# Kernel tuning notes

Measured on AMD Instinct MI355X. Metric: run time of the kernel, lower is better.

## Reference

```python
import jax, jax.numpy as jnp
import numpy as np

N = 100000   # total nodes in batched graph
E = 600000   # total edges
B = 64       # graphs in batch
H = 128      # hidden_dim
A = 64       # action_dim
L = 4        # num mpnn layers
LOG_STD_MIN, LOG_STD_MAX = -20.0, 2.0


def setup_inputs() -> dict:
    key = jax.random.key(0)
    ks = jax.random.split(key, 40)
    s = 0.05

    def w(k, shape):
        return (jax.random.normal(k, shape, jnp.float32) * s)

    inp = {}
    inp["node_feat"] = jax.random.normal(ks[0], (N, 7), jnp.float32)
    inp["edge_feat"] = jax.random.normal(ks[1], (E, 2), jnp.float32)
    # node encoder: Linear(7,H) -> ReLU -> Linear(H,H)
    inp["ne_w1"] = w(ks[2], (7, H)); inp["ne_b1"] = jnp.zeros((H,), jnp.float32)
    inp["ne_w2"] = w(ks[3], (H, H)); inp["ne_b2"] = jnp.zeros((H,), jnp.float32)
    # edge encoder: Linear(2,H) -> ReLU -> Linear(H,H)
    inp["ee_w1"] = w(ks[4], (2, H)); inp["ee_b1"] = jnp.zeros((H,), jnp.float32)
    inp["ee_w2"] = w(ks[5], (H, H)); inp["ee_b2"] = jnp.zeros((H,), jnp.float32)
    # per-layer message net: Linear(3H,H) -> ReLU -> Linear(H,H)  (stacked over L)
    inp["msg_w1"] = w(ks[6], (L, 3 * H, H)); inp["msg_b1"] = jnp.zeros((L, H), jnp.float32)
    inp["msg_w2"] = w(ks[7], (L, H, H));     inp["msg_b2"] = jnp.zeros((L, H), jnp.float32)
    # per-layer update net: Linear(2H,H) -> ReLU -> Linear(H,H)
    inp["upd_w1"] = w(ks[8], (L, 2 * H, H)); inp["upd_b1"] = jnp.zeros((L, H), jnp.float32)
    inp["upd_w2"] = w(ks[9], (L, H, H));     inp["upd_b2"] = jnp.zeros((L, H), jnp.float32)
    # attention-pooling gate: Linear(H,H) -> ReLU -> Linear(H,1)
    inp["gate_w1"] = w(ks[10], (H, H)); inp["gate_b1"] = jnp.zeros((H,), jnp.float32)
    inp["gate_w2"] = w(ks[11], (H, 1)); inp["gate_b2"] = jnp.zeros((1,), jnp.float32)
    # policy net: Linear(H,H) -> ReLU -> Linear(H,H) -> ReLU -> Linear(H,2A)
    inp["pol_w1"] = w(ks[12], (H, H));     inp["pol_b1"] = jnp.zeros((H,), jnp.float32)
    inp["pol_w2"] = w(ks[13], (H, H));     inp["pol_b2"] = jnp.zeros((H,), jnp.float32)
    inp["pol_w3"] = w(ks[14], (H, 2 * A)); inp["pol_b3"] = jnp.zeros((2 * A,), jnp.float32)
    # graph connectivity
    inp["src"] = jax.random.randint(ks[15], (E,), 0, N)
    inp["dst"] = jax.random.randint(ks[16], (E,), 0, N)
    inp["graph_id"] = jnp.sort(jax.random.randint(ks[17], (N,), 0, B))
    return inp


def _mlp2(x, w1, b1, w2, b2):
    return jax.nn.relu(x @ w1 + b1) @ w2 + b2


def reference(node_feat, edge_feat,
              ne_w1, ne_b1, ne_w2, ne_b2,
              ee_w1, ee_b1, ee_w2, ee_b2,
              msg_w1, msg_b1, msg_w2, msg_b2,
              upd_w1, upd_b1, upd_w2, upd_b2,
              gate_w1, gate_b1, gate_w2, gate_b2,
              pol_w1, pol_b1, pol_w2, pol_b2, pol_w3, pol_b3,
              src, dst, graph_id):
    # encode
    h = _mlp2(node_feat, ne_w1, ne_b1, ne_w2, ne_b2)          # [N, H]
    e = _mlp2(edge_feat, ee_w1, ee_b1, ee_w2, ee_b2)          # [E, H]
    # MPNN layers with residual (h = layer(h) + h)
    for l in range(L):
        msg_in = jnp.concatenate([h[src], h[dst], e], axis=1)  # [E, 3H]
        m = _mlp2(msg_in, msg_w1[l], msg_b1[l], msg_w2[l], msg_b2[l])  # [E, H]
        h_agg = jax.ops.segment_sum(m, dst, num_segments=N)    # [N, H]
        upd_in = jnp.concatenate([h, h_agg], axis=1)           # [N, 2H]
        h = _mlp2(upd_in, upd_w1[l], upd_b1[l], upd_w2[l], upd_b2[l]) + h
    # global attention pooling (per-graph segment softmax over gate logits)
    gate = _mlp2(h, gate_w1, gate_b1, gate_w2, gate_b2)[:, 0]  # [N]
    gmax = jax.ops.segment_max(gate, graph_id, num_segments=B)  # [B]
    ex = jnp.exp(gate - gmax[graph_id])                        # [N]
    z = jax.ops.segment_sum(ex, graph_id, num_segments=B)      # [B]
    alpha = ex / z[graph_id]                                   # [N]
    emb = jax.ops.segment_sum(alpha[:, None] * h, graph_id, num_segments=B)  # [B, H]
    # policy head
    out = jax.nn.relu(jax.nn.relu(emb @ pol_w1 + pol_b1) @ pol_w2 + pol_b2) @ pol_w3 + pol_b3  # [B, 2A]
    mean, log_std = out[:, :A], out[:, A:]
    log_std = jnp.clip(log_std, LOG_STD_MIN, LOG_STD_MAX)
    std = jnp.exp(log_std)
    return (mean, std)
```

## Files before the change

kernel.cpp:

```cpp
#include <hip/hip_runtime.h>
#include <stdint.h>

#define NN 100000
#define NE 600000
#define NG 64
#define HD 128
#define HD2 (HD*HD)
#define NLAYER 4
#define SCAN_NB 391
#define NTILES ((NN + 63) / 64)
#define PSLICE 16

typedef unsigned short u16;
typedef unsigned int u32;
typedef unsigned long long u64;
typedef __attribute__((ext_vector_type(8))) short bf16x8;
typedef __attribute__((ext_vector_type(4))) float f32x4;

__device__ __forceinline__ float bf2f(u32 v) { return __uint_as_float(v << 16); }
__device__ __forceinline__ u16 f2bf(float f) {
    u32 u = __float_as_uint(f);
    return (u16)((u + 0x7FFFu + ((u >> 16) & 1u)) >> 16);
}
__device__ __forceinline__ u32 pk2(float a, float b) {
    return (u32)f2bf(a) | ((u32)f2bf(b) << 16);
}

template<bool RELU, bool GATE>
__global__ __launch_bounds__(256, 3) void mgemm_kernel(
    const u16* __restrict__ Xb, const u16* __restrict__ Wt,
    const float* __restrict__ bias, const float* __restrict__ degscale,
    const u16* __restrict__ addend, u16* __restrict__ out, int M,
    const float* __restrict__ gw2, const float* __restrict__ gb2,
    float* __restrict__ gate)
{
    __shared__ u16 WsL[HD * HD];
    __shared__ u16 XsL[64 * HD];
    const int t = threadIdx.x;
    const int lane = t & 63, wave = t >> 6;
    const int cj = ((lane >> 4) << 2);

    for (int i = t; i < HD * 16; i += 256) {
        const int row = i >> 4, c16 = i & 15;
        uint4 v = *(const uint4*)(Wt + (size_t)row * HD + c16 * 8);
        *(uint4*)((char*)WsL + (((row << 8) + (c16 << 4)) ^ ((row & 7) << 4))) = v;
    }
    float4 bcol[8];
    #pragma unroll
    for (int ct = 0; ct < 8; ct++)
        bcol[ct] = bias ? *(const float4*)(bias + ct * 16 + cj)
                        : make_float4(0.f, 0.f, 0.f, 0.f);
    float4 gwv[8];
    if (GATE) {
        #pragma unroll
        for (int ct = 0; ct < 8; ct++)
            gwv[ct] = *(const float4*)(gw2 + ct * 16 + cj);
    }

    const int arow = wave * 16 + (lane & 15);
    const int alin = (arow << 8) + ((lane >> 4) << 4);
    const int axor = (arow & 7) << 4;
    __syncthreads();

    for (int tile = blockIdx.x; tile < NTILES; tile += gridDim.x) {
        const int r0 = tile << 6;
        for (int i = t; i < 64 * 16; i += 256) {
            const int row = i >> 4, c16 = i & 15;
            const int rg = r0 + row;
            uint4 v = make_uint4(0, 0, 0, 0);
            if (rg < M) v = *(const uint4*)(Xb + (size_t)rg * HD + c16 * 8);
            *(uint4*)((char*)XsL + (((row << 8) + (c16 << 4)) ^ ((row & 7) << 4))) = v;
        }
        __syncthreads();

        bf16x8 a[4];
        #pragma unroll
        for (int ks = 0; ks < 4; ks++)
            a[ks] = *(const bf16x8*)((const char*)XsL + ((alin + ks * 64) ^ axor));

        f32x4 acc[8];
        #pragma unroll
        for (int ct = 0; ct < 8; ct++) {
            acc[ct][0] = 0.f; acc[ct][1] = 0.f; acc[ct][2] = 0.f; acc[ct][3] = 0.f;
        }
        #pragma unroll
        for (int ct = 0; ct < 8; ct++) {
            const int bn = ct * 16 + (lane & 15);
            #pragma unroll
            for (int ks = 0; ks < 4; ks++) {
                bf16x8 breg = *(const bf16x8*)((const char*)WsL +
                    (((bn << 8) + ks * 64 + ((lane >> 4) << 4)) ^ ((bn & 7) << 4)));
                acc[ct] = __builtin_amdgcn_mfma_f32_16x16x32_bf16(breg, a[ks], acc[ct], 0, 0, 0);
            }
        }

        const int orow = r0 + wave * 16 + (lane & 15);
        const bool rv = orow < M;
        float gdot = 0.f;
        const float ds = (degscale && rv) ? degscale[orow] : 1.f;
        #pragma unroll
        for (int ct = 0; ct < 8; ct++) {
            const int c0 = ct * 16 + cj;
            float v0 = acc[ct][0], v1 = acc[ct][1], v2 = acc[ct][2], v3 = acc[ct][3];
            if (bias) {
                v0 += bcol[ct].x * ds; v1 += bcol[ct].y * ds;
                v2 += bcol[ct].z * ds; v3 += bcol[ct].w * ds;
            }
            if (addend && rv) {
                ushort4 av = *(const ushort4*)(addend + (size_t)orow * HD + c0);
                v0 += bf2f(av.x); v1 += bf2f(av.y); v2 += bf2f(av.z); v3 += bf2f(av.w);
            }
            if (RELU) {
                v0 = fmaxf(v0, 0.f); v1 = fmaxf(v1, 0.f);
                v2 = fmaxf(v2, 0.f); v3 = fmaxf(v3, 0.f);
            }
            if (GATE) {
                gdot += v0 * gwv[ct].x + v1 * gwv[ct].y + v2 * gwv[ct].z + v3 * gwv[ct].w;
            } else if (rv) {
                ushort4 pk;
                pk.x = f2bf(v0); pk.y = f2bf(v1); pk.z = f2bf(v2); pk.w = f2bf(v3);
                *(ushort4*)(out + (size_t)orow * HD + c0) = pk;
            }
        }
        if (GATE) {
            gdot += __shfl_xor(gdot, 16, 64);
            gdot += __shfl_xor(gdot, 32, 64);
            if ((lane >> 4) == 0 && rv) gate[orow] = gdot + gb2[0];
        }
        __syncthreads();
    }
}

__global__ __launch_bounds__(256, 2) void pqgemm_kernel(
    const u16* __restrict__ Xb, const u16* __restrict__ WtP,
    const u16* __restrict__ WtQ, u16* __restrict__ outP,
    u16* __restrict__ outQ, int M)
{
    __shared__ u16 WsL[2 * HD * HD];
    __shared__ u16 XsL[64 * HD];
    const int t = threadIdx.x;
    const int lane = t & 63, wave = t >> 6;
    const int cj = ((lane >> 4) << 2);

    for (int i = t; i < 2 * HD * 16; i += 256) {
        const int w = i >> 11;
        const int j = i & 2047;
        const int row = j >> 4, c16 = j & 15;
        const u16* Wt = w ? WtQ : WtP;
        uint4 v = *(const uint4*)(Wt + (size_t)row * HD + c16 * 8);
        *(uint4*)((char*)WsL + w * 32768 +
                  (((row << 8) + (c16 << 4)) ^ ((row & 7) << 4))) = v;
    }

    const int arow = wave * 16 + (lane & 15);
    const int alin = (arow << 8) + ((lane >> 4) << 4);
    const int axor = (arow & 7) << 4;
    __syncthreads();

    for (int tile = blockIdx.x; tile < NTILES; tile += gridDim.x) {
        const int r0 = tile << 6;
        for (int i = t; i < 64 * 16; i += 256) {
            const int row = i >> 4, c16 = i & 15;
            const int rg = r0 + row;
            uint4 v = make_uint4(0, 0, 0, 0);
            if (rg < M) v = *(const uint4*)(Xb + (size_t)rg * HD + c16 * 8);
            *(uint4*)((char*)XsL + (((row << 8) + (c16 << 4)) ^ ((row & 7) << 4))) = v;
        }
        __syncthreads();

        bf16x8 a[4];
        #pragma unroll
        for (int ks = 0; ks < 4; ks++)
            a[ks] = *(const bf16x8*)((const char*)XsL + ((alin + ks * 64) ^ axor));

        const int orow = r0 + wave * 16 + (lane & 15);
        const bool rv = orow < M;

        #pragma unroll
        for (int o = 0; o < 2; o++) {
            f32x4 acc[8];
            #pragma unroll
            for (int ct = 0; ct < 8; ct++) {
                acc[ct][0] = 0.f; acc[ct][1] = 0.f; acc[ct][2] = 0.f; acc[ct][3] = 0.f;
            }
            #pragma unroll
            for (int ct = 0; ct < 8; ct++) {
                const int bn = ct * 16 + (lane & 15);
                #pragma unroll
                for (int ks = 0; ks < 4; ks++) {
                    bf16x8 breg = *(const bf16x8*)((const char*)WsL + o * 32768 +
                        (((bn << 8) + ks * 64 + ((lane >> 4) << 4)) ^ ((bn & 7) << 4)));
                    acc[ct] = __builtin_amdgcn_mfma_f32_16x16x32_bf16(breg, a[ks], acc[ct], 0, 0, 0);
                }
            }
            if (rv) {
                u16* out = o ? outQ : outP;
                #pragma unroll
                for (int ct = 0; ct < 8; ct++) {
                    ushort4 pk;
                    pk.x = f2bf(acc[ct][0]); pk.y = f2bf(acc[ct][1]);
                    pk.z = f2bf(acc[ct][2]); pk.w = f2bf(acc[ct][3]);
                    *(ushort4*)(out + (size_t)orow * HD + ct * 16 + cj) = pk;
                }
            }
        }
        __syncthreads();
    }
}

__global__ __launch_bounds__(256, 2) void edge_mfma_kernel(
    const float2* __restrict__ sef, const int* __restrict__ ssrc,
    const int* __restrict__ sdst, const int* __restrict__ off,
    const float* __restrict__ ew1, const float* __restrict__ eb1,
    const u16* __restrict__ Mt, const float* __restrict__ mvec,
    const u16* __restrict__ P, const u16* __restrict__ Q,
    u16* __restrict__ agg)
{
    __shared__ __align__(16) char XHT[HD * 72 * 2];
    __shared__ u16 PsL[64 * 136];
    __shared__ u16 QsL[32 * 136];
    __shared__ u64 dlocL[8];
    __shared__ float ew1L[2 * HD];
    __shared__ float eb1L[HD];
    u16* HT = (u16*)XHT;
    const int t = threadIdx.x, lane = t & 63, wave = t >> 6;
    const int cj = (lane >> 4) << 2;
    const int n0 = blockIdx.x * 32;

    ew1L[t] = ew1[t];
    if (t < HD) eb1L[t] = eb1[t];
    for (int i = t; i < 32 * 32; i += 256) {
        const int row = i >> 5, c4 = (i & 31) * 4;
        *(ushort4*)(QsL + row * 136 + c4) = *(const ushort4*)(Q + (size_t)(n0 + row) * HD + c4);
    }

    float4 mvv[8];
    #pragma unroll
    for (int ct = 0; ct < 8; ct++) mvv[ct] = *(const float4*)(mvec + ct * 16 + cj);

    bf16x8 breg[8][4];
    #pragma unroll
    for (int ct = 0; ct < 8; ct++) {
        const int bn = ct * 16 + (lane & 15);
        #pragma unroll
        for (int ks = 0; ks < 4; ks++)
            breg[ct][ks] = *(const bf16x8*)(Mt + (size_t)bn * HD + ks * 32 + ((lane >> 4) << 3));
    }

    const int rt = wave & 1;
    const int c2b = (wave >> 1) * 4;
    const int nodeid = rt * 16 + (lane & 15);
    f32x4 acc2[4];
    #pragma unroll
    for (int i = 0; i < 4; i++) {
        acc2[i][0] = 0.f; acc2[i][1] = 0.f; acc2[i][2] = 0.f; acc2[i][3] = 0.f;
    }

    const int e0 = off[n0], e1 = off[n0 + 32];
    const int arow = wave * 16 + (lane & 15);
    const int alin = (arow << 8) + ((lane >> 4) << 4);
    const int axor = (arow & 7) << 4;
    const int el = wave * 16 + (lane & 15);
    __syncthreads();

    for (int base = e0; base < e1; base += 64) {
        for (int i = t; i < 64 * 16; i += 256) {
            const int row = i >> 4, c16 = i & 15;
            const int e = base + row;
            uint4 v = make_uint4(0, 0, 0, 0);
            uint4 pvv = make_uint4(0, 0, 0, 0);
            if (e < e1) {
                const float2 f = sef[e];
                const int c8 = c16 * 8;
                float o[8];
                #pragma unroll
                for (int k = 0; k < 8; k++)
                    o[k] = fmaxf(f.x * ew1L[c8 + k] + f.y * ew1L[HD + c8 + k] + eb1L[c8 + k], 0.f);
                v = make_uint4(pk2(o[0], o[1]), pk2(o[2], o[3]), pk2(o[4], o[5]), pk2(o[6], o[7]));
                const int srcI = ssrc[e];
                pvv = *(const uint4*)(P + (size_t)srcI * HD + c16 * 8);
            }
            *(uint4*)(XHT + (((row << 8) + (c16 << 4)) ^ ((row & 7) << 4))) = v;
            *(uint4*)(PsL + row * 136 + c16 * 8) = pvv;
        }
        if (t < 64) {
            const int e = base + t;
            ((unsigned char*)dlocL)[t] = (e < e1) ? (unsigned char)(sdst[e] - n0) : (unsigned char)0xFF;
        }
        __syncthreads();

        bf16x8 a[4];
        #pragma unroll
        for (int ks = 0; ks < 4; ks++)
            a[ks] = *(const bf16x8*)(XHT + ((alin + ks * 64) ^ axor));
        const int e = base + el;
        const bool ev = e < e1;
        const int dl = ev ? (int)((const unsigned char*)dlocL)[el] : 0;
        __syncthreads();

        f32x4 acc[8];
        #pragma unroll
        for (int ct = 0; ct < 8; ct++) {
            acc[ct][0] = 0.f; acc[ct][1] = 0.f; acc[ct][2] = 0.f; acc[ct][3] = 0.f;
        }
        #pragma unroll
        for (int ct = 0; ct < 8; ct++)
            #pragma unroll
            for (int ks = 0; ks < 4; ks++)
                acc[ct] = __builtin_amdgcn_mfma_f32_16x16x32_bf16(breg[ct][ks], a[ks], acc[ct], 0, 0, 0);

        #pragma unroll
        for (int ct = 0; ct < 8; ct++) {
            float v0 = 0.f, v1 = 0.f, v2 = 0.f, v3 = 0.f;
            if (ev) {
                const ushort4 pvc = *(const ushort4*)(PsL + el * 136 + ct * 16 + cj);
                const ushort4 qvc = *(const ushort4*)(QsL + dl * 136 + ct * 16 + cj);
                v0 = fmaxf(acc[ct][0] + bf2f(pvc.x) + bf2f(qvc.x) + mvv[ct].x, 0.f);
                v1 = fmaxf(acc[ct][1] + bf2f(pvc.y) + bf2f(qvc.y) + mvv[ct].y, 0.f);
                v2 = fmaxf(acc[ct][2] + bf2f(pvc.z) + bf2f(qvc.z) + mvv[ct].z, 0.f);
                v3 = fmaxf(acc[ct][3] + bf2f(pvc.w) + bf2f(qvc.w) + mvv[ct].w, 0.f);
            }
            const int c0 = ct * 16 + cj;
            HT[(c0 + 0) * 72 + el] = f2bf(v0);
            HT[(c0 + 1) * 72 + el] = f2bf(v1);
            HT[(c0 + 2) * 72 + el] = f2bf(v2);
            HT[(c0 + 3) * 72 + el] = f2bf(v3);
        }
        __syncthreads();

        #pragma unroll
        for (int ks2 = 0; ks2 < 2; ks2++) {
            const u64 dv = dlocL[ks2 * 4 + (lane >> 4)];
            bf16x8 sfrag;
            #pragma unroll
            for (int j = 0; j < 8; j++) {
                const int dvj = (int)((dv >> (8 * j)) & 0xFF);
                sfrag[j] = (dvj == nodeid) ? (short)0x3F80 : (short)0;
            }
            #pragma unroll
            for (int i = 0; i < 4; i++) {
                const int col = (c2b + i) * 16 + (lane & 15);
                bf16x8 hfrag = *(const bf16x8*)(HT + col * 72 + ks2 * 32 + ((lane >> 4) << 3));
                acc2[i] = __builtin_amdgcn_mfma_f32_16x16x32_bf16(sfrag, hfrag, acc2[i], 0, 0, 0);
            }
        }
        __syncthreads();
    }

    u16* BNC = (u16*)XHT;
    #pragma unroll
    for (int i = 0; i < 4; i++) {
        const int col = (c2b + i) * 16 + (lane & 15);
        #pragma unroll
        for (int r = 0; r < 4; r++) {
            const int nl = rt * 16 + ((lane >> 4) << 2) + r;
            BNC[nl * 136 + col] = f2bf(acc2[i][r]);
        }
    }
    __syncthreads();
    for (int i = t; i < 32 * 16; i += 256) {
        const int row = i >> 4, c16 = i & 15;
        *(uint4*)(agg + (size_t)(n0 + row) * HD + c16 * 8) =
            *(const uint4*)(BNC + row * 136 + c16 * 8);
    }
}

__global__ __launch_bounds__(256) void gemm128_kernel(
    const float* __restrict__ X, const float* __restrict__ W,
    float* __restrict__ out, int M)
{
    __shared__ float Ws[HD * HD];
    __shared__ float Xs[32 * HD];
    const int t = threadIdx.x;
    for (int i = t; i < HD * HD / 4; i += 256)
        ((float4*)Ws)[i] = ((const float4*)W)[i];
    const int c0 = (t & 31) * 4;
    const int rb = (t >> 5) * 4;
    __syncthreads();
    const int ntiles = M / 32;
    for (int tile = blockIdx.x; tile < ntiles; tile += gridDim.x) {
        const int r0 = tile * 32;
        const float4* xg = (const float4*)(X + (size_t)r0 * HD);
        for (int i = t; i < 32 * HD / 4; i += 256)
            ((float4*)Xs)[i] = xg[i];
        __syncthreads();
        float acc[4][4];
        #pragma unroll
        for (int a = 0; a < 4; a++)
            #pragma unroll
            for (int b = 0; b < 4; b++) acc[a][b] = 0.f;
        for (int k = 0; k < HD; k += 4) {
            float4 w0 = *(const float4*)(Ws + (k + 0) * HD + c0);
            float4 w1 = *(const float4*)(Ws + (k + 1) * HD + c0);
            float4 w2 = *(const float4*)(Ws + (k + 2) * HD + c0);
            float4 w3 = *(const float4*)(Ws + (k + 3) * HD + c0);
            #pragma unroll
            for (int rr = 0; rr < 4; rr++) {
                float4 xv = *(const float4*)(Xs + (rb + rr) * HD + k);
                acc[rr][0] += xv.x * w0.x + xv.y * w1.x + xv.z * w2.x + xv.w * w3.x;
                acc[rr][1] += xv.x * w0.y + xv.y * w1.y + xv.z * w2.y + xv.w * w3.y;
                acc[rr][2] += xv.x * w0.z + xv.y * w1.z + xv.z * w2.z + xv.w * w3.z;
                acc[rr][3] += xv.x * w0.w + xv.y * w1.w + xv.z * w2.w + xv.w * w3.w;
            }
        }
        #pragma unroll
        for (int rr = 0; rr < 4; rr++) {
            const int row = r0 + rb + rr;
            *(float4*)(out + (size_t)row * HD + c0) =
                make_float4(acc[rr][0], acc[rr][1], acc[rr][2], acc[rr][3]);
        }
        __syncthreads();
    }
}

__global__ void mvec_kernel(const float* __restrict__ eb2,
                            const float* __restrict__ W1c,
                            const float* __restrict__ mb1,
                            float* __restrict__ out) {
    const int j = threadIdx.x;
    if (j < HD) {
        float s = mb1[j];
        for (int i = 0; i < HD; i++) s += eb2[i] * W1c[(size_t)i * HD + j];
        out[j] = s;
    }
}

__global__ __launch_bounds__(256) void wprep_kernel(
    const float* __restrict__ msg_w1, const float* __restrict__ msg_w2,
    const float* __restrict__ upd_w1, const float* __restrict__ upd_w2,
    const float* __restrict__ gw1, const float* __restrict__ ne_w2,
    const float* __restrict__ Mw, u16* __restrict__ wt)
{
    __shared__ float tileL[HD * (HD + 1)];
    const int b = blockIdx.x, t = threadIdx.x;
    const int l = b & 3;
    const float* S;
    if (b < 4)       S = msg_w1 + (size_t)l * 3 * HD2;
    else if (b < 8)  S = msg_w1 + (size_t)l * 3 * HD2 + HD2;
    else if (b < 12) S = Mw + (size_t)l * HD2;
    else if (b < 16) S = msg_w2 + (size_t)l * HD2;
    else if (b < 20) S = upd_w1 + (size_t)l * 2 * HD2;
    else if (b < 24) S = upd_w1 + (size_t)l * 2 * HD2 + HD2;
    else if (b < 28) S = upd_w2 + (size_t)l * HD2;
    else if (b == 28) S = gw1;
    else             S = ne_w2;
    u16* D = wt + (size_t)b * HD2;
    for (int i = t; i < HD2; i += 256) {
        const int k = i >> 7, n = i & 127;
        tileL[k * (HD + 1) + n] = S[i];
    }
    __syncthreads();
    for (int i = t; i < HD2; i += 256) {
        const int n = i >> 7, k = i & 127;
        D[i] = f2bf(tileL[k * (HD + 1) + n]);
    }
}

__global__ __launch_bounds__(256) void ne1_kernel(
    const float* __restrict__ nf, const float* __restrict__ w1,
    const float* __restrict__ b1, u16* __restrict__ out)
{
    __shared__ float w1s[7 * HD];
    __shared__ float b1s[HD];
    const int t = threadIdx.x;
    for (int i = t; i < 7 * HD; i += 256) w1s[i] = w1[i];
    if (t < HD) b1s[t] = b1[t];
    __syncthreads();
    const int row = blockIdx.x * 32 + (t >> 3);
    const int c0 = (t & 7) * 16;
    if (row < NN) {
        float f[7];
        #pragma unroll
        for (int k = 0; k < 7; k++) f[k] = nf[(size_t)row * 7 + k];
        float o[16];
        #pragma unroll
        for (int c = 0; c < 16; c++) {
            float a = b1s[c0 + c];
            #pragma unroll
            for (int k = 0; k < 7; k++) a += f[k] * w1s[k * HD + c0 + c];
            o[c] = fmaxf(a, 0.f);
        }
        uint4 v0 = make_uint4(pk2(o[0], o[1]), pk2(o[2], o[3]), pk2(o[4], o[5]), pk2(o[6], o[7]));
        uint4 v1 = make_uint4(pk2(o[8], o[9]), pk2(o[10], o[11]), pk2(o[12], o[13]), pk2(o[14], o[15]));
        *(uint4*)(out + (size_t)row * HD + c0) = v0;
        *(uint4*)(out + (size_t)row * HD + c0 + 8) = v1;
    }
}

__global__ void deg_count_kernel(const int* __restrict__ dst, int* __restrict__ deg) {
    const int i = blockIdx.x * 256 + threadIdx.x;
    if (i < NE) atomicAdd(&deg[dst[i]], 1);
}
__global__ void scan1_kernel(const int* __restrict__ deg, int* __restrict__ part) {
    __shared__ int s[256];
    const int t = threadIdx.x, i = blockIdx.x * 256 + t;
    s[t] = (i < NN) ? deg[i] : 0;
    __syncthreads();
    for (int d = 128; d > 0; d >>= 1) { if (t < d) s[t] += s[t + d]; __syncthreads(); }
    if (t == 0) part[blockIdx.x] = s[0];
}
__global__ void scan2_kernel(int* __restrict__ part, int nb) {
    if (threadIdx.x == 0 && blockIdx.x == 0) {
        int run = 0;
        for (int b = 0; b < nb; b++) { const int v = part[b]; part[b] = run; run += v; }
    }
}
__global__ void scan3_kernel(const int* __restrict__ deg, const int* __restrict__ part,
                             int* __restrict__ off, int* __restrict__ pos) {
    __shared__ int s[256];
    const int t = threadIdx.x, i = blockIdx.x * 256 + t;
    const int v = (i < NN) ? deg[i] : 0;
    s[t] = v;
    __syncthreads();
    for (int d = 1; d < 256; d <<= 1) {
        const int x = (t >= d) ? s[t - d] : 0;
        __syncthreads();
        s[t] += x;
        __syncthreads();
    }
    const int excl = s[t] - v + part[blockIdx.x];
    if (i < NN) {
        off[i] = excl; pos[i] = excl;
        if (i == NN - 1) off[NN] = excl + v;
    }
}
__global__ void scatter_kernel(const int* __restrict__ src, const int* __restrict__ dst,
                               const float* __restrict__ ef, int* __restrict__ pos,
                               float2* __restrict__ sef, int* __restrict__ ssrc,
                               int* __restrict__ sdst) {
    const int e = blockIdx.x * 256 + threadIdx.x;
    if (e < NE) {
        const int d = dst[e];
        const int p = atomicAdd(&pos[d], 1);
        sef[p] = make_float2(ef[2 * e], ef[2 * e + 1]);
        ssrc[p] = src[e]; sdst[p] = d;
    }
}
__global__ void degf_kernel(const int* __restrict__ off, float* __restrict__ degf) {
    const int n = blockIdx.x * 256 + threadIdx.x;
    if (n < NN) degf[n] = (float)(off[n + 1] - off[n]);
}

__global__ void bounds_kernel(const int* __restrict__ gid, int* __restrict__ gs) {
    const int g = threadIdx.x;
    if (g <= NG) {
        int lo = 0, hi = NN;
        while (lo < hi) {
            const int mid = (lo + hi) >> 1;
            if (gid[mid] < g) lo = mid + 1; else hi = mid;
        }
        gs[g] = lo;
    }
}

__global__ __launch_bounds__(256) void poolA_kernel(
    const float* __restrict__ gate, const int* __restrict__ gs,
    float* __restrict__ ex, float* __restrict__ gz)
{
    __shared__ float red[256];
    const int g = blockIdx.x, t = threadIdx.x;
    const int s = gs[g], e = gs[g + 1];
    if (s >= e) {
        if (t == 0) gz[g] = 1.f;
        return;
    }
    float m = -3.4e38f;
    for (int i = s + t; i < e; i += 256) m = fmaxf(m, gate[i]);
    red[t] = m; __syncthreads();
    for (int d = 128; d > 0; d >>= 1) {
        if (t < d) red[t] = fmaxf(red[t], red[t + d]);
        __syncthreads();
    }
    const float gm = red[0];
    __syncthreads();
    float zs = 0.f;
    for (int i = s + t; i < e; i += 256) {
        const float ev = expf(gate[i] - gm);
        ex[i] = ev; zs += ev;
    }
    red[t] = zs; __syncthreads();
    for (int d = 128; d > 0; d >>= 1) {
        if (t < d) red[t] += red[t + d];
        __syncthreads();
    }
    if (t == 0) gz[g] = red[0];
}

__global__ __launch_bounds__(256) void poolB_kernel(
    const float* __restrict__ ex, const int* __restrict__ gs,
    const u16* __restrict__ hb, float* __restrict__ partial)
{
    __shared__ float redL[16][132];
    const int b = blockIdx.x;
    const int g = b / PSLICE, sl = b % PSLICE;
    const int lo = gs[g], hi = gs[g + 1];
    const int len = hi - lo;
    const int chunk = (len + PSLICE - 1) / PSLICE;
    const int ns = lo + sl * chunk;
    const int ne = min(ns + chunk, hi);
    const int t = threadIdx.x;
    const int c8 = (t & 15) * 8;
    const int ro = t >> 4;
    float acc[8] = {0.f, 0.f, 0.f, 0.f, 0.f, 0.f, 0.f, 0.f};
    for (int n = ns + ro; n < ne; n += 16) {
        const float w = ex[n];
        const ushort4 h0 = *(const ushort4*)(hb + (size_t)n * HD + c8);
        const ushort4 h1 = *(const ushort4*)(hb + (size_t)n * HD + c8 + 4);
        acc[0] += w * bf2f(h0.x); acc[1] += w * bf2f(h0.y);
        acc[2] += w * bf2f(h0.z); acc[3] += w * bf2f(h0.w);
        acc[4] += w * bf2f(h1.x); acc[5] += w * bf2f(h1.y);
        acc[6] += w * bf2f(h1.z); acc[7] += w * bf2f(h1.w);
    }
    #pragma unroll
    for (int j = 0; j < 8; j++) redL[ro][c8 + j] = acc[j];
    __syncthreads();
    if (t < HD) {
        float s = 0.f;
        #pragma unroll
        for (int r = 0; r < 16; r++) s += redL[r][t];
        partial[(size_t)b * HD + t] = s;
    }
}

__global__ void poolC_kernel(const float* __restrict__ partial,
                             const float* __restrict__ gz,
                             float* __restrict__ emb)
{
    const int g = blockIdx.x, t = threadIdx.x;
    float s = 0.f;
    #pragma unroll
    for (int sl = 0; sl < PSLICE; sl++)
        s += partial[(size_t)(g * PSLICE + sl) * HD + t];
    emb[(size_t)g * HD + t] = s / gz[g];
}

__global__ __launch_bounds__(256) void policy_kernel(
    const float* __restrict__ emb,
    const float* __restrict__ w1, const float* __restrict__ b1,
    const float* __restrict__ w2, const float* __restrict__ b2,
    const float* __restrict__ w3, const float* __restrict__ b3,
    float* __restrict__ out)
{
    __shared__ float A[NG * HD];
    __shared__ float Bs[NG * HD];
    const int t = threadIdx.x;
    for (int i = t; i < NG * HD / 4; i += 256)
        ((float4*)A)[i] = ((const float4*)emb)[i];
    __syncthreads();
    const int c0 = (t & 31) * 4;
    const int rb = (t >> 5) * 8;
    {
        float4 bv = *(const float4*)(b1 + c0);
        for (int rr = 0; rr < 8; rr++) {
            const int r = rb + rr;
            float a0 = bv.x, a1 = bv.y, a2 = bv.z, a3 = bv.w;
            for (int k = 0; k < HD; k++) {
                const float x = A[r * HD + k];
                float4 wv = *(const float4*)(w1 + k * HD + c0);
                a0 += x * wv.x; a1 += x * wv.y; a2 += x * wv.z; a3 += x * wv.w;
            }
            *(float4*)(Bs + r * HD + c0) =
                make_float4(fmaxf(a0, 0.f), fmaxf(a1, 0.f), fmaxf(a2, 0.f), fmaxf(a3, 0.f));
        }
    }
    __syncthreads();
    {
        float4 bv = *(const float4*)(b2 + c0);
        for (int rr = 0; rr < 8; rr++) {
            const int r = rb + rr;
            float a0 = bv.x, a1 = bv.y, a2 = bv.z, a3 = bv.w;
            for (int k = 0; k < HD; k++) {
                const float x = Bs[r * HD + k];
                float4 wv = *(const float4*)(w2 + k * HD + c0);
                a0 += x * wv.x; a1 += x * wv.y; a2 += x * wv.z; a3 += x * wv.w;
            }
            *(float4*)(A + r * HD + c0) =
                make_float4(fmaxf(a0, 0.f), fmaxf(a1, 0.f), fmaxf(a2, 0.f), fmaxf(a3, 0.f));
        }
    }
    __syncthreads();
    {
        float4 bv = *(const float4*)(b3 + c0);
        for (int rr = 0; rr < 8; rr++) {
            const int r = rb + rr;
            float a[4] = {bv.x, bv.y, bv.z, bv.w};
            for (int k = 0; k < HD; k++) {
                const float x = A[r * HD + k];
                float4 wv = *(const float4*)(w3 + k * HD + c0);
                a[0] += x * wv.x; a[1] += x * wv.y; a[2] += x * wv.z; a[3] += x * wv.w;
            }
            #pragma unroll
            for (int j = 0; j < 4; j++) {
                const int c = c0 + j;
                if (c < 64) {
                    out[r * 64 + c] = a[j];
                } else {
                    const float ls = fminf(fmaxf(a[j], -20.f), 2.f);
                    out[4096 + r * 64 + (c - 64)] = expf(ls);
                }
            }
        }
    }
}

extern "C" void kernel_launch(void* const* d_in, const int* in_sizes, int n_in,
                              void* d_out, int out_size, void* d_ws, size_t ws_size,
                              hipStream_t stream) {
    const float* node_feat = (const float*)d_in[0];
    const float* edge_feat = (const float*)d_in[1];
    const float* ne_w1 = (const float*)d_in[2];
    const float* ne_b1 = (const float*)d_in[3];
    const float* ne_w2 = (const float*)d_in[4];
    const float* ne_b2 = (const float*)d_in[5];
    const float* ee_w1 = (const float*)d_in[6];
    const float* ee_b1 = (const float*)d_in[7];
    const float* ee_w2 = (const float*)d_in[8];
    const float* ee_b2 = (const float*)d_in[9];
    const float* msg_w1 = (const float*)d_in[10];
    const float* msg_b1 = (const float*)d_in[11];
    const float* msg_w2 = (const float*)d_in[12];
    const float* msg_b2 = (const float*)d_in[13];
    const float* upd_w1 = (const float*)d_in[14];
    const float* upd_b1 = (const float*)d_in[15];
    const float* upd_w2 = (const float*)d_in[16];
    const float* upd_b2 = (const float*)d_in[17];
    const float* gate_w1 = (const float*)d_in[18];
    const float* gate_b1 = (const float*)d_in[19];
    const float* gate_w2 = (const float*)d_in[20];
    const float* gate_b2 = (const float*)d_in[21];
    const float* pol_w1 = (const float*)d_in[22];
    const float* pol_b1 = (const float*)d_in[23];
    const float* pol_w2 = (const float*)d_in[24];
    const float* pol_b2 = (const float*)d_in[25];
    const float* pol_w3 = (const float*)d_in[26];
    const float* pol_b3 = (const float*)d_in[27];
    const int* src = (const int*)d_in[28];
    const int* dst = (const int*)d_in[29];
    const int* gid = (const int*)d_in[30];

    char* p = (char*)d_ws;
    u16* hb   = (u16*)p;    p += (size_t)NN * HD * 2;
    u16* Pb   = (u16*)p;    p += (size_t)NN * HD * 2;
    u16* Qb   = (u16*)p;    p += (size_t)NN * HD * 2;
    u16* aggb = (u16*)p;    p += (size_t)NN * HD * 2;
    float2* sef = (float2*)p; p += (size_t)NE * 8;
    int* ssrc = (int*)p;    p += (size_t)NE * 4;
    int* sdst = (int*)p;    p += (size_t)NE * 4;
    int* off  = (int*)p;    p += (size_t)(NN + 4) * 4;
    int* pos  = (int*)p;    p += (size_t)NN * 4;
    int* deg  = (int*)p;    p += (size_t)NN * 4;
    float* degf = (float*)p; p += (size_t)NN * 4;
    float* gate = (float*)p; p += (size_t)NN * 4;
    float* ex   = (float*)p; p += (size_t)NN * 4;
    int* part = (int*)p;    p += 2048;
    int* gs   = (int*)p;    p += 512;
    float* gz   = (float*)p; p += 256;
    float* emb = (float*)p; p += (size_t)NG * HD * 4;
    float* partialP = (float*)p; p += (size_t)NG * PSLICE * HD * 4;
    float* Mw = (float*)p;  p += (size_t)NLAYER * HD2 * 4;
    float* mvec = (float*)p; p += (size_t)NLAYER * HD * 4;
    u16* wt = (u16*)p;      p += (size_t)30 * HD2 * 2;

    hipMemsetAsync(deg, 0, (size_t)NN * 4, stream);
    deg_count_kernel<<<(NE + 255) / 256, 256, 0, stream>>>(dst, deg);
    scan1_kernel<<<SCAN_NB, 256, 0, stream>>>(deg, part);
    scan2_kernel<<<1, 64, 0, stream>>>(part, SCAN_NB);
    scan3_kernel<<<SCAN_NB, 256, 0, stream>>>(deg, part, off, pos);
    degf_kernel<<<SCAN_NB, 256, 0, stream>>>(off, degf);
    scatter_kernel<<<(NE + 255) / 256, 256, 0, stream>>>(src, dst, edge_feat, pos, sef, ssrc, sdst);
    bounds_kernel<<<1, 128, 0, stream>>>(gid, gs);

    for (int l = 0; l < NLAYER; l++) {
        const float* W1c = msg_w1 + (size_t)l * 3 * HD2 + 2 * HD2;
        gemm128_kernel<<<4, 256, 0, stream>>>(ee_w2, W1c, Mw + (size_t)l * HD2, HD);
        mvec_kernel<<<1, 128, 0, stream>>>(ee_b2, W1c, msg_b1 + (size_t)l * HD,
                                           mvec + (size_t)l * HD);
    }
    wprep_kernel<<<30, 256, 0, stream>>>(msg_w1, msg_w2, upd_w1, upd_w2, gate_w1, ne_w2, Mw, wt);

    ne1_kernel<<<3125, 256, 0, stream>>>(node_feat, ne_w1, ne_b1, Pb);
    mgemm_kernel<false, false><<<512, 256, 0, stream>>>(
        Pb, wt + (size_t)29 * HD2, ne_b2, nullptr, nullptr, hb, NN, nullptr, nullptr, nullptr);

    for (int l = 0; l < NLAYER; l++) {
        pqgemm_kernel<<<512, 256, 0, stream>>>(
            hb, wt + (size_t)(0 + l) * HD2, wt + (size_t)(4 + l) * HD2, Pb, Qb, NN);
        edge_mfma_kernel<<<NN / 32, 256, 0, stream>>>(sef, ssrc, sdst, off, ee_w1, ee_b1,
            wt + (size_t)(8 + l) * HD2, mvec + (size_t)l * HD, Pb, Qb, aggb);
        mgemm_kernel<false, false><<<512, 256, 0, stream>>>(
            aggb, wt + (size_t)(12 + l) * HD2, msg_b2 + (size_t)l * HD, degf, nullptr, Pb, NN,
            nullptr, nullptr, nullptr);
        mgemm_kernel<false, false><<<512, 256, 0, stream>>>(
            hb, wt + (size_t)(16 + l) * HD2, nullptr, nullptr, nullptr, Qb, NN,
            nullptr, nullptr, nullptr);
        mgemm_kernel<true, false><<<512, 256, 0, stream>>>(
            Pb, wt + (size_t)(20 + l) * HD2, upd_b1 + (size_t)l * HD, nullptr, Qb, aggb, NN,
            nullptr, nullptr, nullptr);
        mgemm_kernel<false, false><<<512, 256, 0, stream>>>(
            aggb, wt + (size_t)(24 + l) * HD2, upd_b2 + (size_t)l * HD, nullptr, hb, hb, NN,
            nullptr, nullptr, nullptr);
    }

    mgemm_kernel<true, true><<<512, 256, 0, stream>>>(
        hb, wt + (size_t)28 * HD2, gate_b1, nullptr, nullptr, nullptr, NN,
        gate_w2, gate_b2, gate);
    poolA_kernel<<<NG, 256, 0, stream>>>(gate, gs, ex, gz);
    poolB_kernel<<<NG * PSLICE, 256, 0, stream>>>(ex, gs, hb, partialP);
    poolC_kernel<<<NG, 128, 0, stream>>>(partialP, gz, emb);
    policy_kernel<<<1, 256, 0, stream>>>(emb, pol_w1, pol_b1, pol_w2, pol_b2, pol_w3, pol_b3, (float*)d_out);
}
```

Before: 1.451 ms.

## Fold message second linear into update first linear to drop a node GEMM

After: 1.430 ms. About the same (-1.4%).

```diff
diff --git a/kernel.cpp b/kernel.cpp
--- a/kernel.cpp
+++ b/kernel.cpp
@@ -413,20 +413,20 @@
     }
 }
 
-__global__ void mvec_kernel(const float* __restrict__ eb2,
-                            const float* __restrict__ W1c,
+__global__ void mvec_kernel(const float* __restrict__ vec,
+                            const float* __restrict__ W,
                             const float* __restrict__ mb1,
                             float* __restrict__ out) {
     const int j = threadIdx.x;
     if (j < HD) {
-        float s = mb1[j];
-        for (int i = 0; i < HD; i++) s += eb2[i] * W1c[(size_t)i * HD + j];
+        float s = mb1 ? mb1[j] : 0.f;
+        for (int i = 0; i < HD; i++) s += vec[i] * W[(size_t)i * HD + j];
         out[j] = s;
     }
 }
 
 __global__ __launch_bounds__(256) void wprep_kernel(
-    const float* __restrict__ msg_w1, const float* __restrict__ msg_w2,
+    const float* __restrict__ msg_w1, const float* __restrict__ Mw2,
     const float* __restrict__ upd_w1, const float* __restrict__ upd_w2,
     const float* __restrict__ gw1, const float* __restrict__ ne_w2,
     const float* __restrict__ Mw, u16* __restrict__ wt)
@@ -438,7 +438,7 @@
     if (b < 4)       S = msg_w1 + (size_t)l * 3 * HD2;
     else if (b < 8)  S = msg_w1 + (size_t)l * 3 * HD2 + HD2;
     else if (b < 12) S = Mw + (size_t)l * HD2;
-    else if (b < 16) S = msg_w2 + (size_t)l * HD2;
+    else if (b < 16) S = Mw2 + (size_t)l * HD2;
     else if (b < 20) S = upd_w1 + (size_t)l * 2 * HD2;
     else if (b < 24) S = upd_w1 + (size_t)l * 2 * HD2 + HD2;
     else if (b < 28) S = upd_w2 + (size_t)l * HD2;
@@ -757,8 +757,10 @@
     float* gz   = (float*)p; p += 256;
     float* emb = (float*)p; p += (size_t)NG * HD * 4;
     float* partialP = (float*)p; p += (size_t)NG * PSLICE * HD * 4;
-    float* Mw = (float*)p;  p += (size_t)NLAYER * HD2 * 4;
+    float* Mw  = (float*)p; p += (size_t)NLAYER * HD2 * 4;
+    float* Mw2 = (float*)p; p += (size_t)NLAYER * HD2 * 4;
     float* mvec = (float*)p; p += (size_t)NLAYER * HD * 4;
+    float* b2u  = (float*)p; p += (size_t)NLAYER * HD * 4;
     u16* wt = (u16*)p;      p += (size_t)30 * HD2 * 2;
 
     hipMemsetAsync(deg, 0, (size_t)NN * 4, stream);
@@ -772,11 +774,16 @@
 
     for (int l = 0; l < NLAYER; l++) {
         const float* W1c = msg_w1 + (size_t)l * 3 * HD2 + 2 * HD2;
+        const float* U1b = upd_w1 + (size_t)l * 2 * HD2 + HD2;
         gemm128_kernel<<<4, 256, 0, stream>>>(ee_w2, W1c, Mw + (size_t)l * HD2, HD);
         mvec_kernel<<<1, 128, 0, stream>>>(ee_b2, W1c, msg_b1 + (size_t)l * HD,
                                            mvec + (size_t)l * HD);
-    }
-    wprep_kernel<<<30, 256, 0, stream>>>(msg_w1, msg_w2, upd_w1, upd_w2, gate_w1, ne_w2, Mw, wt);
+        gemm128_kernel<<<4, 256, 0, stream>>>(msg_w2 + (size_t)l * HD2, U1b,
+                                              Mw2 + (size_t)l * HD2, HD);
+        mvec_kernel<<<1, 128, 0, stream>>>(msg_b2 + (size_t)l * HD, U1b, nullptr,
+                                           b2u + (size_t)l * HD);
+    }
+    wprep_kernel<<<30, 256, 0, stream>>>(msg_w1, Mw2, upd_w1, upd_w2, gate_w1, ne_w2, Mw, wt);
 
     ne1_kernel<<<3125, 256, 0, stream>>>(node_feat, ne_w1, ne_b1, Pb);
     mgemm_kernel<false, false><<<512, 256, 0, stream>>>(
@@ -788,16 +795,13 @@
         edge_mfma_kernel<<<NN / 32, 256, 0, stream>>>(sef, ssrc, sdst, off, ee_w1, ee_b1,
             wt + (size_t)(8 + l) * HD2, mvec + (size_t)l * HD, Pb, Qb, aggb);
         mgemm_kernel<false, false><<<512, 256, 0, stream>>>(
-            aggb, wt + (size_t)(12 + l) * HD2, msg_b2 + (size_t)l * HD, degf, nullptr, Pb, NN,
+            hb, wt + (size_t)(16 + l) * HD2, upd_b1 + (size_t)l * HD, nullptr, nullptr, Qb, NN,
+            nullptr, nullptr, nullptr);
+        mgemm_kernel<true, false><<<512, 256, 0, stream>>>(
+            aggb, wt + (size_t)(12 + l) * HD2, b2u + (size_t)l * HD, degf, Qb, Pb, NN,
             nullptr, nullptr, nullptr);
         mgemm_kernel<false, false><<<512, 256, 0, stream>>>(
-            hb, wt + (size_t)(16 + l) * HD2, nullptr, nullptr, nullptr, Qb, NN,
-            nullptr, nullptr, nullptr);
-        mgemm_kernel<true, false><<<512, 256, 0, stream>>>(
-            Pb, wt + (size_t)(20 + l) * HD2, upd_b1 + (size_t)l * HD, nullptr, Qb, aggb, NN,
-            nullptr, nullptr, nullptr);
-        mgemm_kernel<false, false><<<512, 256, 0, stream>>>(
-            aggb, wt + (size_t)(24 + l) * HD2, upd_b2 + (size_t)l * HD, nullptr, hb, hb, NN,
+            Pb, wt + (size_t)(24 + l) * HD2, upd_b2 + (size_t)l * HD, nullptr, hb, hb, NN,
             nullptr, nullptr, nullptr);
     }
 
```
